# Performance work log

Measured on AMD Instinct MI355X. Metric: run time of the kernel, lower is better.

## Reference

```python
import jax, jax.numpy as jnp
import numpy as np

N = 8192
E = 131072
IN = 512
H = 8
C = 128
HC = H * C
EPS = 1e-5
NEG_SLOPE = 0.2


def _gatv2(x, src, dst, Wl, bl, Wr, br, att, bias):
    """GATv2Conv (PyG semantics, concat=True, self-loops already in src/dst)."""
    n = x.shape[0]
    xl = (x @ Wl + bl).reshape(n, H, C)  # source transform (lin_l)
    xr = (x @ Wr + br).reshape(n, H, C)  # dest transform (lin_r)
    m = xl[src] + xr[dst]                # [E,H,C] per-edge message
    e = jnp.einsum('ehc,hc->eh', jax.nn.leaky_relu(m, NEG_SLOPE), att)  # [E,H]
    # segment softmax over destination nodes
    emax = jax.ops.segment_max(e, dst, num_segments=n)
    w = jnp.exp(e - emax[dst])
    denom = jax.ops.segment_sum(w, dst, num_segments=n)
    alpha = w / denom[dst]               # [E,H]
    out = jax.ops.segment_sum(alpha[:, :, None] * xl[src], dst, num_segments=n)
    return out.reshape(n, HC) + bias


def _bn(x, gamma, beta):
    mu = jnp.mean(x, axis=0)
    var = jnp.mean((x - mu) ** 2, axis=0)
    return (x - mu) * jax.lax.rsqrt(var + EPS) * gamma + beta


def setup_inputs() -> dict:
    key = jax.random.key(0)
    ks = jax.random.split(key, 16)
    s = 0.05
    return {
        'x': jax.random.normal(ks[0], (N, IN), jnp.float32),
        'edge_index': jax.random.randint(ks[1], (2, E), 0, N, jnp.int32),
        'W1l': jax.random.normal(ks[2], (IN, HC), jnp.float32) * s,
        'b1l': jnp.zeros((HC,), jnp.float32),
        'W1r': jax.random.normal(ks[3], (IN, HC), jnp.float32) * s,
        'b1r': jnp.zeros((HC,), jnp.float32),
        'att1': jax.random.normal(ks[4], (H, C), jnp.float32) * s,
        'bias1': jnp.zeros((HC,), jnp.float32),
        'g1': jnp.ones((HC,), jnp.float32),
        'beta1': jnp.zeros((HC,), jnp.float32),
        'W2l': jax.random.normal(ks[5], (HC, HC), jnp.float32) * s,
        'b2l': jnp.zeros((HC,), jnp.float32),
        'W2r': jax.random.normal(ks[6], (HC, HC), jnp.float32) * s,
        'b2r': jnp.zeros((HC,), jnp.float32),
        'att2': jax.random.normal(ks[7], (H, C), jnp.float32) * s,
        'bias2': jnp.zeros((HC,), jnp.float32),
        'g2': jnp.ones((HC,), jnp.float32),
        'beta2': jnp.zeros((HC,), jnp.float32),
    }


def reference(x, edge_index, W1l, b1l, W1r, b1r, att1, bias1, g1, beta1,
              W2l, b2l, W2r, b2r, att2, bias2, g2, beta2):
    n = x.shape[0]
    loops = jnp.arange(n, dtype=edge_index.dtype)
    src = jnp.concatenate([edge_index[0], loops])
    dst = jnp.concatenate([edge_index[1], loops])
    h = _gatv2(x, src, dst, W1l, b1l, W1r, b1r, att1, bias1)
    h = jax.nn.elu(_bn(h, g1, beta1))
    h = _gatv2(h, src, dst, W2l, b2l, W2r, b2r, att2, bias2)
    h = jax.nn.elu(_bn(h, g2, beta2))
    return h
```

## Files before the change

kernel.cpp:

```cpp
#include <hip/hip_runtime.h>
#include <stdint.h>

#define NN     8192
#define NEDGE  131072
#define NETOT  (NEDGE + NN)
#define K_IN   512
#define HC_    1024
#define NOUT   2048
#define BNEPS  1e-5f
#define SLOPE  0.2f

typedef __bf16 bf16x8 __attribute__((ext_vector_type(8)));
typedef float  f32x4  __attribute__((ext_vector_type(4)));

__device__ __forceinline__ float bf2f(unsigned short u) {
  union { uint32_t u; float f; } c; c.u = ((uint32_t)u) << 16; return c.f;
}
__device__ __forceinline__ unsigned short f2bf(float f) {
  union { float f; uint32_t u; } c; c.f = f;
  uint32_t r = c.u + 0x7fffu + ((c.u >> 16) & 1u);
  return (unsigned short)(r >> 16);
}
__device__ __forceinline__ void unpack2(uint32_t u, float& lo, float& hi) {
  union { uint32_t u; float f; } a, b;
  a.u = u << 16; b.u = u & 0xffff0000u;
  lo = a.f; hi = b.f;
}

__device__ __forceinline__ void gload16(const void* g, void* l) {
  __builtin_amdgcn_global_load_lds(
      (const __attribute__((address_space(1))) uint32_t*)g,
      (__attribute__((address_space(3))) uint32_t*)l, 16, 0, 0);
}

__global__ __launch_bounds__(256) void k_cvt_bf16(const float* __restrict__ in,
                                                  unsigned short* __restrict__ out, int n4) {
  int i = blockIdx.x * 256 + threadIdx.x;
  if (i >= n4) return;
  float4 v = *(const float4*)&in[(size_t)i * 4];
  ushort4 o;
  o.x = f2bf(v.x); o.y = f2bf(v.y); o.z = f2bf(v.z); o.w = f2bf(v.w);
  *(ushort4*)&out[(size_t)i * 4] = o;
}

__global__ __launch_bounds__(256) void k_transpose_bf16(const float* __restrict__ W,
                                                        unsigned short* __restrict__ Wt,
                                                        int K, int N) {
  __shared__ float tile[32][33];
  int n0 = blockIdx.x * 32, k0 = blockIdx.y * 32;
  int tx = threadIdx.x & 31, ty = threadIdx.x >> 5;
  for (int i = ty; i < 32; i += 8)
    tile[i][tx] = W[(size_t)(k0 + i) * N + n0 + tx];
  __syncthreads();
  for (int i = ty; i < 32; i += 8)
    Wt[(size_t)(n0 + i) * K + k0 + tx] = f2bf(tile[tx][i]);
}

__global__ __launch_bounds__(256) void k_hist(const int* __restrict__ ei, int* __restrict__ cnt) {
  int i = blockIdx.x * 256 + threadIdx.x;
  if (i >= NETOT) return;
  int d = (i < NEDGE) ? ei[NEDGE + i] : (i - NEDGE);
  atomicAdd(&cnt[d], 1);
}

__global__ __launch_bounds__(256) void k_scan(const int* __restrict__ cnt,
                                              int* __restrict__ rowptr,
                                              int* __restrict__ cursor) {
  __shared__ int part[256];
  int t = threadIdx.x;
  int base = t * 32;
  int s = 0;
  for (int i = 0; i < 32; ++i) s += cnt[base + i];
  part[t] = s;
  __syncthreads();
  for (int off = 1; off < 256; off <<= 1) {
    int u = (t >= off) ? part[t - off] : 0;
    __syncthreads();
    part[t] += u;
    __syncthreads();
  }
  int run = part[t] - s;
  for (int i = 0; i < 32; ++i) {
    rowptr[base + i] = run;
    cursor[base + i] = run;
    run += cnt[base + i];
  }
  if (t == 255) rowptr[NN] = run;
}

__global__ __launch_bounds__(256) void k_scatter(const int* __restrict__ ei,
                                                 int* __restrict__ cursor,
                                                 int* __restrict__ srcs) {
  int i = blockIdx.x * 256 + threadIdx.x;
  if (i >= NETOT) return;
  int s, d;
  if (i < NEDGE) { s = ei[i]; d = ei[NEDGE + i]; }
  else           { s = d = i - NEDGE; }
  int pos = atomicAdd(&cursor[d], 1);
  srcs[pos] = s;
}

__global__ __launch_bounds__(512, 2) void k_gemm256(const unsigned short* __restrict__ A,
                                                    const unsigned short* __restrict__ Bt,
                                                    const float* __restrict__ biasL,
                                                    const float* __restrict__ biasR,
                                                    unsigned short* __restrict__ C,
                                                    int K) {
  __shared__ unsigned short lA[2][256 * 64];
  __shared__ unsigned short lB[2][256 * 64];

  const int bid = blockIdx.x;
  const int xcd = bid & 7, idx = bid >> 3;
  const int m0 = (xcd * 4 + (idx & 3)) * 256;
  const int n0 = (idx >> 2) * 256;

  const int tid = threadIdx.x;
  const int l   = tid & 63;
  const int wv  = tid >> 6;
  const int wm  = wv >> 2, wn = wv & 3;
  const int l15 = l & 15, l4 = l >> 4;

  const int row0 = tid >> 3;
  const int sgk  = (tid & 7) ^ (row0 & 7);
  const size_t aoff0 = (size_t)(m0 + row0) * K + sgk * 8;
  const size_t boff0 = (size_t)(n0 + row0) * K + sgk * 8;
  const int ldsch = tid * 8;

  const f32x4 vzero = {0.f, 0.f, 0.f, 0.f};
  f32x4 acc[8][4];
#pragma unroll
  for (int i = 0; i < 8; ++i)
#pragma unroll
    for (int j = 0; j < 4; ++j) acc[i][j] = vzero;

  auto stage = [&](int kt, int buf) {
    const int k0 = kt * 64;
#pragma unroll
    for (int i = 0; i < 4; ++i)
      gload16(&A[aoff0 + (size_t)i * 64 * K + k0], &lA[buf][ldsch + i * 4096]);
#pragma unroll
    for (int i = 0; i < 4; ++i)
      gload16(&Bt[boff0 + (size_t)i * 64 * K + k0], &lB[buf][ldsch + i * 4096]);
  };

  auto compute = [&](int buf) {
    __builtin_amdgcn_s_setprio(1);
#pragma unroll
    for (int kk = 0; kk < 2; ++kk) {
      bf16x8 af[8], bfr[4];
#pragma unroll
      for (int f = 0; f < 8; ++f) {
        int r = wm * 128 + f * 16 + l15;
        int g = (kk * 4 + l4) ^ (r & 7);
        af[f] = *(const bf16x8*)&lA[buf][r * 64 + g * 8];
      }
#pragma unroll
      for (int f = 0; f < 4; ++f) {
        int r = wn * 64 + f * 16 + l15;
        int g = (kk * 4 + l4) ^ (r & 7);
        bfr[f] = *(const bf16x8*)&lB[buf][r * 64 + g * 8];
      }
#pragma unroll
      for (int fm = 0; fm < 8; ++fm)
#pragma unroll
        for (int fn = 0; fn < 4; ++fn)
          acc[fm][fn] = __builtin_amdgcn_mfma_f32_16x16x32_bf16(af[fm], bfr[fn], acc[fm][fn], 0, 0, 0);
    }
    __builtin_amdgcn_s_setprio(0);
  };

  const int NT = K >> 6;
  stage(0, 0);
  stage(1, 1);
  int cur = 0;
  for (int kt = 0; kt < NT - 1; ++kt) {
    asm volatile("s_waitcnt vmcnt(8)" ::: "memory");
    __builtin_amdgcn_s_barrier();
    asm volatile("" ::: "memory");
    compute(cur);
    asm volatile("" ::: "memory");
    __builtin_amdgcn_s_barrier();
    asm volatile("" ::: "memory");
    if (kt < NT - 2) stage(kt + 2, cur);
    cur ^= 1;
  }
  asm volatile("s_waitcnt vmcnt(0)" ::: "memory");
  __builtin_amdgcn_s_barrier();
  asm volatile("" ::: "memory");
  compute(cur);

  const float* bias = (n0 < HC_) ? biasL : (biasR - HC_);
#pragma unroll
  for (int fm = 0; fm < 8; ++fm) {
#pragma unroll
    for (int fn = 0; fn < 4; ++fn) {
      int col = n0 + wn * 64 + fn * 16 + l15;
      float bv = bias[col];
#pragma unroll
      for (int j = 0; j < 4; ++j) {
        int row = m0 + wm * 128 + fm * 16 + l4 * 4 + j;
        C[(size_t)row * NOUT + col] = f2bf(acc[fm][fn][j] + bv);
      }
    }
  }
}

__global__ __launch_bounds__(256) void k_edge_agg(const unsigned short* __restrict__ XLR,
                                                  const float* __restrict__ att,
                                                  const float* __restrict__ bias,
                                                  const int* __restrict__ rowptr,
                                                  const int* __restrict__ srcs,
                                                  float* __restrict__ out) {
  const int d   = blockIdx.x;
  const int tid = threadIdx.x;
  const int g   = tid >> 6;
  const int l   = tid & 63;
  const int c0  = l * 16;

  float attv[16], xrv[16];
  {
    const float4* ap = (const float4*)&att[c0];
#pragma unroll
    for (int q = 0; q < 4; ++q) {
      float4 v = ap[q];
      attv[q * 4 + 0] = v.x; attv[q * 4 + 1] = v.y;
      attv[q * 4 + 2] = v.z; attv[q * 4 + 3] = v.w;
    }
    const uint4* rp = (const uint4*)&XLR[(size_t)d * NOUT + HC_ + c0];
    uint4 u0 = rp[0], u1 = rp[1];
    unpack2(u0.x, xrv[0], xrv[1]);  unpack2(u0.y, xrv[2], xrv[3]);
    unpack2(u0.z, xrv[4], xrv[5]);  unpack2(u0.w, xrv[6], xrv[7]);
    unpack2(u1.x, xrv[8], xrv[9]);  unpack2(u1.y, xrv[10], xrv[11]);
    unpack2(u1.z, xrv[12], xrv[13]); unpack2(u1.w, xrv[14], xrv[15]);
  }

  float acc[16];
#pragma unroll
  for (int j = 0; j < 16; ++j) acc[j] = 0.f;
  float den = 0.f;

  const int beg = rowptr[d], end = rowptr[d + 1];
  for (int i = beg + g; i < end; i += 4) {
    const int s = srcs[i];
    const uint4* rp = (const uint4*)&XLR[(size_t)s * NOUT + c0];
    uint4 u0 = rp[0], u1 = rp[1];
    float x[16];
    unpack2(u0.x, x[0], x[1]);   unpack2(u0.y, x[2], x[3]);
    unpack2(u0.z, x[4], x[5]);   unpack2(u0.w, x[6], x[7]);
    unpack2(u1.x, x[8], x[9]);   unpack2(u1.y, x[10], x[11]);
    unpack2(u1.z, x[12], x[13]); unpack2(u1.w, x[14], x[15]);
    float p = 0.f;
#pragma unroll
    for (int j = 0; j < 16; ++j) {
      float m  = x[j] + xrv[j];
      float lr = fmaxf(m, SLOPE * m);
      p = fmaf(lr, attv[j], p);
    }
    p += __shfl_xor(p, 1);
    p += __shfl_xor(p, 2);
    p += __shfl_xor(p, 4);
    float wgt = __expf(p);
    den += wgt;
#pragma unroll
    for (int j = 0; j < 16; ++j) acc[j] = fmaf(wgt, x[j], acc[j]);
  }

  __shared__ float sacc[4][64][17];
  __shared__ float sden[4][64];
#pragma unroll
  for (int j = 0; j < 16; ++j) sacc[g][l][j] = acc[j];
  sden[g][l] = den;
  __syncthreads();

  const int c  = tid * 4;
  const int hl = (c >> 7) * 8;
  float dtot = sden[0][hl] + sden[1][hl] + sden[2][hl] + sden[3][hl];
  float inv  = 1.0f / dtot;
  float4 bv  = *(const float4*)&bias[c];
  float o[4];
#pragma unroll
  for (int j = 0; j < 4; ++j) {
    int cc = c + j, ll = cc >> 4, jj = cc & 15;
    float s = sacc[0][ll][jj] + sacc[1][ll][jj] + sacc[2][ll][jj] + sacc[3][ll][jj];
    o[j] = s * inv;
  }
  float4 ov = {o[0] + bv.x, o[1] + bv.y, o[2] + bv.z, o[3] + bv.w};
  *(float4*)&out[(size_t)d * HC_ + c] = ov;
}

__global__ __launch_bounds__(256) void k_colstats(const float* __restrict__ X,
                                                  float* __restrict__ stats) {
  int col = blockIdx.x * 256 + threadIdx.x;
  int r0 = blockIdx.y * 128;
  float s = 0.f, q = 0.f;
  for (int r = r0; r < r0 + 128; ++r) {
    float v = X[(size_t)r * HC_ + col];
    s += v;
    q += v * v;
  }
  atomicAdd(&stats[col], s);
  atomicAdd(&stats[HC_ + col], q);
}

template <bool OUT_BF16>
__global__ __launch_bounds__(256) void k_bn_elu(const float* __restrict__ X,
                                                const float* __restrict__ stats,
                                                const float* __restrict__ gamma,
                                                const float* __restrict__ beta,
                                                void* __restrict__ outp) {
  size_t idx = (size_t)blockIdx.x * 256 + threadIdx.x;
  size_t e0 = idx * 4;
  int col = (int)(e0 & (HC_ - 1));
  float4 xv = *(const float4*)&X[e0];
  float xs[4] = {xv.x, xv.y, xv.z, xv.w};
  float os[4];
  const float rn = 1.0f / (float)NN;
#pragma unroll
  for (int j = 0; j < 4; ++j) {
    int c = col + j;
    float mu = stats[c] * rn;
    float var = stats[HC_ + c] * rn - mu * mu;
    float v = (xs[j] - mu) * rsqrtf(var + BNEPS) * gamma[c] + beta[c];
    os[j] = v > 0.f ? v : (__expf(v) - 1.f);
  }
  if (OUT_BF16) {
    ushort4 o;
    o.x = f2bf(os[0]); o.y = f2bf(os[1]); o.z = f2bf(os[2]); o.w = f2bf(os[3]);
    *(ushort4*)&((unsigned short*)outp)[e0] = o;
  } else {
    float4 o = {os[0], os[1], os[2], os[3]};
    *(float4*)&((float*)outp)[e0] = o;
  }
}

extern "C" void kernel_launch(void* const* d_in, const int* in_sizes, int n_in,
                              void* d_out, int out_size, void* d_ws, size_t ws_size,
                              hipStream_t stream) {
  const float* x     = (const float*)d_in[0];
  const int*   ei    = (const int*)d_in[1];
  const float* W1l   = (const float*)d_in[2];
  const float* b1l   = (const float*)d_in[3];
  const float* W1r   = (const float*)d_in[4];
  const float* b1r   = (const float*)d_in[5];
  const float* att1  = (const float*)d_in[6];
  const float* bias1 = (const float*)d_in[7];
  const float* g1    = (const float*)d_in[8];
  const float* be1   = (const float*)d_in[9];
  const float* W2l   = (const float*)d_in[10];
  const float* b2l   = (const float*)d_in[11];
  const float* W2r   = (const float*)d_in[12];
  const float* b2r   = (const float*)d_in[13];
  const float* att2  = (const float*)d_in[14];
  const float* bias2 = (const float*)d_in[15];
  const float* g2    = (const float*)d_in[16];
  const float* be2   = (const float*)d_in[17];
  float* out = (float*)d_out;

  char* wsb = (char*)d_ws;
  size_t o = 0;
  auto alloc = [&](size_t b) {
    void* p = wsb + o;
    o = (o + b + 255) & ~(size_t)255;
    return p;
  };
  unsigned short* xbf  = (unsigned short*)alloc((size_t)NN * K_IN * 2);
  unsigned short* wT1  = (unsigned short*)alloc((size_t)NOUT * K_IN * 2);
  unsigned short* wT2  = (unsigned short*)alloc((size_t)NOUT * HC_ * 2);
  unsigned short* XLR  = (unsigned short*)alloc((size_t)NN * NOUT * 2);
  unsigned short* h1bf = (unsigned short*)alloc((size_t)NN * HC_ * 2);
  int* cnt     = (int*)alloc((size_t)NN * 4);
  int* rowptr  = (int*)alloc((size_t)(NN + 1) * 4);
  int* cursor  = (int*)alloc((size_t)NN * 4);
  int* srcs    = (int*)alloc((size_t)NETOT * 4);
  float* stats = (float*)alloc((size_t)2 * HC_ * 4);

  hipMemsetAsync(cnt, 0, (size_t)NN * 4, stream);
  hipMemsetAsync(stats, 0, (size_t)2 * HC_ * 4, stream);

  k_cvt_bf16<<<(NN * K_IN / 4 + 255) / 256, 256, 0, stream>>>(x, xbf, NN * K_IN / 4);
  k_transpose_bf16<<<dim3(HC_ / 32, K_IN / 32), 256, 0, stream>>>(W1l, wT1, K_IN, HC_);
  k_transpose_bf16<<<dim3(HC_ / 32, K_IN / 32), 256, 0, stream>>>(W1r, wT1 + (size_t)HC_ * K_IN, K_IN, HC_);
  k_transpose_bf16<<<dim3(HC_ / 32, HC_ / 32), 256, 0, stream>>>(W2l, wT2, HC_, HC_);
  k_transpose_bf16<<<dim3(HC_ / 32, HC_ / 32), 256, 0, stream>>>(W2r, wT2 + (size_t)HC_ * HC_, HC_, HC_);

  k_hist<<<(NETOT + 255) / 256, 256, 0, stream>>>(ei, cnt);
  k_scan<<<1, 256, 0, stream>>>(cnt, rowptr, cursor);
  k_scatter<<<(NETOT + 255) / 256, 256, 0, stream>>>(ei, cursor, srcs);

  k_gemm256<<<256, 512, 0, stream>>>(xbf, wT1, b1l, b1r, XLR, K_IN);
  k_edge_agg<<<NN, 256, 0, stream>>>(XLR, att1, bias1, rowptr, srcs, out);
  k_colstats<<<dim3(HC_ / 256, NN / 128), 256, 0, stream>>>(out, stats);
  k_bn_elu<true><<<NN * HC_ / 4 / 256, 256, 0, stream>>>(out, stats, g1, be1, h1bf);

  k_gemm256<<<256, 512, 0, stream>>>(h1bf, wT2, b2l, b2r, XLR, HC_);
  k_edge_agg<<<NN, 256, 0, stream>>>(XLR, att2, bias2, rowptr, srcs, out);
  hipMemsetAsync(stats, 0, (size_t)2 * HC_ * 4, stream);
  k_colstats<<<dim3(HC_ / 256, NN / 128), 256, 0, stream>>>(out, stats);
  k_bn_elu<false><<<NN * HC_ / 4 / 256, 256, 0, stream>>>(out, stats, g2, be2, out);
}
```

Before: 253.3 us.

## Interleave GEMM staging with quadrant compute and vectorize edge aggregation

The GEMM main loop is split into four quadrant MFMA phases, with global-to-LDS loads for the next k-tile issued in halves between them. This overlaps memory traffic with compute at a finer grain, at the cost of many more barriers. The edge aggregation kernel now uses packed f32x2 arithmetic, aiming at packed FMA/max instructions. It also prefetches the next neighbour's row one iteration ahead to hide gather latency, which raises register pressure.

```diff
diff --git a/kernel.cpp b/kernel.cpp
--- a/kernel.cpp
+++ b/kernel.cpp
@@ -12,6 +12,7 @@
 
 typedef __bf16 bf16x8 __attribute__((ext_vector_type(8)));
 typedef float  f32x4  __attribute__((ext_vector_type(4)));
+typedef float  f32x2  __attribute__((ext_vector_type(2)));
 
 __device__ __forceinline__ float bf2f(unsigned short u) {
   union { uint32_t u; float f; } c; c.u = ((uint32_t)u) << 16; return c.f;
@@ -21,10 +22,10 @@
   uint32_t r = c.u + 0x7fffu + ((c.u >> 16) & 1u);
   return (unsigned short)(r >> 16);
 }
-__device__ __forceinline__ void unpack2(uint32_t u, float& lo, float& hi) {
+__device__ __forceinline__ f32x2 upk2(uint32_t u) {
   union { uint32_t u; float f; } a, b;
   a.u = u << 16; b.u = u & 0xffff0000u;
-  lo = a.f; hi = b.f;
+  f32x2 r; r.x = a.f; r.y = b.f; return r;
 }
 
 __device__ __forceinline__ void gload16(const void* g, void* l) {
@@ -32,6 +33,8 @@
       (const __attribute__((address_space(1))) uint32_t*)g,
       (__attribute__((address_space(3))) uint32_t*)l, 16, 0, 0);
 }
+
+#define SBAR() do { asm volatile("" ::: "memory"); __builtin_amdgcn_s_barrier(); asm volatile("" ::: "memory"); } while (0)
 
 __global__ __launch_bounds__(256) void k_cvt_bf16(const float* __restrict__ in,
                                                   unsigned short* __restrict__ out, int n4) {
@@ -120,11 +123,8 @@
   const int wm  = wv >> 2, wn = wv & 3;
   const int l15 = l & 15, l4 = l >> 4;
 
-  const int row0 = tid >> 3;
-  const int sgk  = (tid & 7) ^ (row0 & 7);
-  const size_t aoff0 = (size_t)(m0 + row0) * K + sgk * 8;
-  const size_t boff0 = (size_t)(n0 + row0) * K + sgk * 8;
-  const int ldsch = tid * 8;
+  const int srow = tid >> 3;
+  const int ssgk = (tid & 7) ^ (srow & 7);
 
   const f32x4 vzero = {0.f, 0.f, 0.f, 0.f};
   f32x4 acc[8][4];
@@ -133,61 +133,86 @@
 #pragma unroll
     for (int j = 0; j < 4; ++j) acc[i][j] = vzero;
 
-  auto stage = [&](int kt, int buf) {
-    const int k0 = kt * 64;
-#pragma unroll
-    for (int i = 0; i < 4; ++i)
-      gload16(&A[aoff0 + (size_t)i * 64 * K + k0], &lA[buf][ldsch + i * 4096]);
-#pragma unroll
-    for (int i = 0; i < 4; ++i)
-      gload16(&Bt[boff0 + (size_t)i * 64 * K + k0], &lB[buf][ldsch + i * 4096]);
-  };
-
-  auto compute = [&](int buf) {
+  bf16x8 a2[8];
+  bf16x8 bb[2][4];
+
+  auto stageA = [&](int kt, int h) {
+    const int buf = kt & 1;
+    const size_t go = (size_t)(m0 + h * 128 + srow) * K + (size_t)kt * 64 + ssgk * 8;
+    unsigned short* lp = &lA[buf][h * 8192 + tid * 8];
+    gload16(&A[go], lp);
+    gload16(&A[go + (size_t)64 * K], lp + 4096);
+  };
+  auto stageB = [&](int kt, int h) {
+    const int buf = kt & 1;
+    const size_t go = (size_t)(n0 + h * 128 + srow) * K + (size_t)kt * 64 + ssgk * 8;
+    unsigned short* lp = &lB[buf][h * 8192 + tid * 8];
+    gload16(&Bt[go], lp);
+    gload16(&Bt[go + (size_t)64 * K], lp + 4096);
+  };
+  auto readA = [&](int buf, int qm) {
+#pragma unroll
+    for (int fm = 0; fm < 4; ++fm)
+#pragma unroll
+      for (int kk = 0; kk < 2; ++kk) {
+        int r = wm * 128 + (qm * 4 + fm) * 16 + l15;
+        int g = (kk * 4 + l4) ^ (r & 7);
+        a2[fm * 2 + kk] = *(const bf16x8*)&lA[buf][r * 64 + g * 8];
+      }
+  };
+  auto readB = [&](int buf, int qn) {
+#pragma unroll
+    for (int fn = 0; fn < 2; ++fn)
+#pragma unroll
+      for (int kk = 0; kk < 2; ++kk) {
+        int r = wn * 64 + (qn * 2 + fn) * 16 + l15;
+        int g = (kk * 4 + l4) ^ (r & 7);
+        bb[qn][fn * 2 + kk] = *(const bf16x8*)&lB[buf][r * 64 + g * 8];
+      }
+  };
+  auto quad = [&](int qm, int qn) {
     __builtin_amdgcn_s_setprio(1);
 #pragma unroll
-    for (int kk = 0; kk < 2; ++kk) {
-      bf16x8 af[8], bfr[4];
-#pragma unroll
-      for (int f = 0; f < 8; ++f) {
-        int r = wm * 128 + f * 16 + l15;
-        int g = (kk * 4 + l4) ^ (r & 7);
-        af[f] = *(const bf16x8*)&lA[buf][r * 64 + g * 8];
-      }
-#pragma unroll
-      for (int f = 0; f < 4; ++f) {
-        int r = wn * 64 + f * 16 + l15;
-        int g = (kk * 4 + l4) ^ (r & 7);
-        bfr[f] = *(const bf16x8*)&lB[buf][r * 64 + g * 8];
-      }
-#pragma unroll
-      for (int fm = 0; fm < 8; ++fm)
-#pragma unroll
-        for (int fn = 0; fn < 4; ++fn)
-          acc[fm][fn] = __builtin_amdgcn_mfma_f32_16x16x32_bf16(af[fm], bfr[fn], acc[fm][fn], 0, 0, 0);
-    }
+    for (int fm = 0; fm < 4; ++fm)
+#pragma unroll
+      for (int fn = 0; fn < 2; ++fn)
+#pragma unroll
+        for (int kk = 0; kk < 2; ++kk)
+          acc[qm * 4 + fm][qn * 2 + fn] = __builtin_amdgcn_mfma_f32_16x16x32_bf16(
+              a2[fm * 2 + kk], bb[qn][fn * 2 + kk], acc[qm * 4 + fm][qn * 2 + fn], 0, 0, 0);
     __builtin_amdgcn_s_setprio(0);
   };
 
   const int NT = K >> 6;
-  stage(0, 0);
-  stage(1, 1);
-  int cur = 0;
-  for (int kt = 0; kt < NT - 1; ++kt) {
-    asm volatile("s_waitcnt vmcnt(8)" ::: "memory");
-    __builtin_amdgcn_s_barrier();
-    asm volatile("" ::: "memory");
-    compute(cur);
-    asm volatile("" ::: "memory");
-    __builtin_amdgcn_s_barrier();
-    asm volatile("" ::: "memory");
-    if (kt < NT - 2) stage(kt + 2, cur);
-    cur ^= 1;
-  }
-  asm volatile("s_waitcnt vmcnt(0)" ::: "memory");
-  __builtin_amdgcn_s_barrier();
-  asm volatile("" ::: "memory");
-  compute(cur);
+
+  stageA(0, 0); stageA(0, 1); stageB(0, 0); stageB(0, 1);
+  if (NT > 1) stageA(1, 0);
+  asm volatile("s_waitcnt vmcnt(2)" ::: "memory");
+  SBAR();
+
+  for (int t = 0; t < NT; ++t) {
+    const int buf = t & 1;
+    readA(buf, 0); readB(buf, 0);
+    if (t + 1 < NT) stageA(t + 1, 1);
+    SBAR();
+    quad(0, 0);
+    SBAR();
+    readB(buf, 1);
+    if (t + 1 < NT) stageB(t + 1, 0);
+    SBAR();
+    quad(0, 1);
+    SBAR();
+    readA(buf, 1);
+    if (t + 1 < NT) stageB(t + 1, 1);
+    SBAR();
+    quad(1, 0);
+    SBAR();
+    if (t + 2 < NT) stageA(t + 2, 0);
+    asm volatile("s_waitcnt vmcnt(2)" ::: "memory");
+    SBAR();
+    quad(1, 1);
+    SBAR();
+  }
 
   const float* bias = (n0 < HC_) ? biasL : (biasR - HC_);
 #pragma unroll
@@ -217,58 +242,65 @@
   const int l   = tid & 63;
   const int c0  = l * 16;
 
-  float attv[16], xrv[16];
+  f32x2 attv[8], xrv[8];
   {
-    const float4* ap = (const float4*)&att[c0];
-#pragma unroll
-    for (int q = 0; q < 4; ++q) {
-      float4 v = ap[q];
-      attv[q * 4 + 0] = v.x; attv[q * 4 + 1] = v.y;
-      attv[q * 4 + 2] = v.z; attv[q * 4 + 3] = v.w;
-    }
+    const f32x2* ap = (const f32x2*)&att[c0];
+#pragma unroll
+    for (int q = 0; q < 8; ++q) attv[q] = ap[q];
     const uint4* rp = (const uint4*)&XLR[(size_t)d * NOUT + HC_ + c0];
     uint4 u0 = rp[0], u1 = rp[1];
-    unpack2(u0.x, xrv[0], xrv[1]);  unpack2(u0.y, xrv[2], xrv[3]);
-    unpack2(u0.z, xrv[4], xrv[5]);  unpack2(u0.w, xrv[6], xrv[7]);
-    unpack2(u1.x, xrv[8], xrv[9]);  unpack2(u1.y, xrv[10], xrv[11]);
-    unpack2(u1.z, xrv[12], xrv[13]); unpack2(u1.w, xrv[14], xrv[15]);
-  }
-
-  float acc[16];
-#pragma unroll
-  for (int j = 0; j < 16; ++j) acc[j] = 0.f;
+    xrv[0] = upk2(u0.x); xrv[1] = upk2(u0.y); xrv[2] = upk2(u0.z); xrv[3] = upk2(u0.w);
+    xrv[4] = upk2(u1.x); xrv[5] = upk2(u1.y); xrv[6] = upk2(u1.z); xrv[7] = upk2(u1.w);
+  }
+
+  f32x2 acc2[8];
+#pragma unroll
+  for (int j = 0; j < 8; ++j) acc2[j] = (f32x2){0.f, 0.f};
   float den = 0.f;
 
   const int beg = rowptr[d], end = rowptr[d + 1];
-  for (int i = beg + g; i < end; i += 4) {
-    const int s = srcs[i];
-    const uint4* rp = (const uint4*)&XLR[(size_t)s * NOUT + c0];
-    uint4 u0 = rp[0], u1 = rp[1];
-    float x[16];
-    unpack2(u0.x, x[0], x[1]);   unpack2(u0.y, x[2], x[3]);
-    unpack2(u0.z, x[4], x[5]);   unpack2(u0.w, x[6], x[7]);
-    unpack2(u1.x, x[8], x[9]);   unpack2(u1.y, x[10], x[11]);
-    unpack2(u1.z, x[12], x[13]); unpack2(u1.w, x[14], x[15]);
-    float p = 0.f;
-#pragma unroll
-    for (int j = 0; j < 16; ++j) {
-      float m  = x[j] + xrv[j];
-      float lr = fmaxf(m, SLOPE * m);
-      p = fmaf(lr, attv[j], p);
+  int i = beg + g;
+  uint4 u0n, u1n;
+  if (i < end) {
+    const uint4* rp = (const uint4*)&XLR[(size_t)srcs[i] * NOUT + c0];
+    u0n = rp[0]; u1n = rp[1];
+  }
+  while (i < end) {
+    uint4 u0 = u0n, u1 = u1n;
+    int nx = i + 4;
+    if (nx < end) {
+      const uint4* rp = (const uint4*)&XLR[(size_t)srcs[nx] * NOUT + c0];
+      u0n = rp[0]; u1n = rp[1];
     }
+    f32x2 x[8];
+    x[0] = upk2(u0.x); x[1] = upk2(u0.y); x[2] = upk2(u0.z); x[3] = upk2(u0.w);
+    x[4] = upk2(u1.x); x[5] = upk2(u1.y); x[6] = upk2(u1.z); x[7] = upk2(u1.w);
+    f32x2 ps = (f32x2){0.f, 0.f};
+#pragma unroll
+    for (int j = 0; j < 8; ++j) {
+      f32x2 m  = x[j] + xrv[j];
+      f32x2 lr = __builtin_elementwise_max(m, m * SLOPE);
+      ps = lr * attv[j] + ps;
+    }
+    float p = ps.x + ps.y;
     p += __shfl_xor(p, 1);
     p += __shfl_xor(p, 2);
     p += __shfl_xor(p, 4);
     float wgt = __expf(p);
     den += wgt;
-#pragma unroll
-    for (int j = 0; j < 16; ++j) acc[j] = fmaf(wgt, x[j], acc[j]);
+    f32x2 w2 = (f32x2){wgt, wgt};
+#pragma unroll
+    for (int j = 0; j < 8; ++j) acc2[j] = w2 * x[j] + acc2[j];
+    i = nx;
   }
 
   __shared__ float sacc[4][64][17];
   __shared__ float sden[4][64];
 #pragma unroll
-  for (int j = 0; j < 16; ++j) sacc[g][l][j] = acc[j];
+  for (int j = 0; j < 8; ++j) {
+    sacc[g][l][j * 2]     = acc2[j].x;
+    sacc[g][l][j * 2 + 1] = acc2[j].y;
+  }
   sden[g][l] = den;
   __syncthreads();
 
```

New measurement: 252.1 us. About the same (-0.5%).
